# Kernel optimization log

Hardware: AMD Instinct MI355X
Metric: run time of the kernel (lower is better)

Reference implementation:

```python
import jax, jax.numpy as jnp
import numpy as np

HEADS = 8


def setup_inputs() -> dict:
    key = jax.random.key(0)
    k1, k2, k3, k4, k5 = jax.random.split(key, 5)
    bt, b_sz, n, dim = 2, 4, 1024, 512
    inner6 = 3072  # inner_dim * 6 where inner_dim = heads * dim_head = 512
    return {
        "x": jax.random.normal(k1, (bt, b_sz, n, dim), dtype=jnp.float32),
        "W_qkv": jax.random.normal(k2, (dim, inner6), dtype=jnp.float32) * 0.02,
        "b_qkv": jax.random.normal(k3, (inner6,), dtype=jnp.float32) * 0.02,
        "W_out": jax.random.normal(k4, (1024, dim), dtype=jnp.float32) * 0.02,
        "b_out": jax.random.normal(k5, (dim,), dtype=jnp.float32) * 0.02,
    }


def reference(x, W_qkv, b_qkv, W_out, b_out):
    bt, b_sz, n, dim = x.shape
    # to_qkv: Linear(dim, 3072) -> reshape (bt,b,n,3,H,hd) -> transpose(2,4)
    qkv = (x @ W_qkv + b_qkv).reshape(bt, b_sz, n, 3, HEADS, -1)
    qkv = qkv.transpose(0, 1, 4, 3, 2, 5)  # (bt, b, H, 3, n, hd)
    q, k, v = qkv[:, :, :, 0], qkv[:, :, :, 1], qkv[:, :, :, 2]
    scale = (dim // HEADS) ** -0.5  # faithful: uses dim//heads, not per-head width
    attn = jax.nn.softmax(jnp.einsum("abhnd,abhmd->abhnm", q * scale, k), axis=-1)
    out = jnp.einsum("abhnm,abhmd->abhnd", attn, v)
    out = out.transpose(0, 1, 3, 2, 4).reshape(bt, b_sz, n, -1)  # (bt,b,n,H*hd)
    return out @ W_out + b_out
```

## Files before the change

### kernel.cpp

```cpp
#include <hip/hip_runtime.h>

typedef __attribute__((ext_vector_type(4))) float f32x4;
typedef __attribute__((ext_vector_type(16))) float f32x16;
typedef __attribute__((ext_vector_type(8))) __bf16 bf16x8;
typedef __attribute__((ext_vector_type(8))) unsigned short ushortx8;
typedef unsigned short u16;
typedef unsigned int u32;

#define AS1 __attribute__((address_space(1)))
#define AS3 __attribute__((address_space(3)))

__device__ __forceinline__ void gld_lds16(const void* g, void* s) {
  __builtin_amdgcn_global_load_lds((AS1 void*)g, (AS3 void*)s, 16, 0, 0);
}

__device__ __forceinline__ u16 f2bf(float f) {
  unsigned int u = __float_as_uint(f);
  unsigned int r = (u + 0x7FFFu + ((u >> 16) & 1u)) >> 16;
  return (u16)r;
}

#define QSCALE 0.1803368801111244f

__global__ void cvt_f32_bf16(const float* __restrict__ src, u16* __restrict__ dst, int n) {
  int i = (blockIdx.x * blockDim.x + threadIdx.x) * 8;
  if (i >= n) return;
  const float4 a = *(const float4*)&src[i];
  const float4 b = *(const float4*)&src[i + 4];
  ushortx8 o;
  o[0] = f2bf(a.x); o[1] = f2bf(a.y); o[2] = f2bf(a.z); o[3] = f2bf(a.w);
  o[4] = f2bf(b.x); o[5] = f2bf(b.y); o[6] = f2bf(b.z); o[7] = f2bf(b.w);
  *(ushortx8*)&dst[i] = o;
}

__global__ void scale_bias(const float* __restrict__ src, float* __restrict__ dst, int n,
                           int boundary, float s) {
  int i = blockIdx.x * blockDim.x + threadIdx.x;
  if (i < n) dst[i] = src[i] * (i < boundary ? s : 1.0f);
}

__global__ void transpose_to_bf16(const float* __restrict__ src, u16* __restrict__ dst,
                                  int R, int C, int boundary, float s) {
  __shared__ float tile[32][33];
  const int c0 = blockIdx.x * 32, r0 = blockIdx.y * 32;
  const int tx = threadIdx.x, ty = threadIdx.y;
  #pragma unroll
  for (int i = ty; i < 32; i += 8)
    tile[i][tx] = src[(size_t)(r0 + i) * C + c0 + tx];
  __syncthreads();
  #pragma unroll
  for (int i = ty; i < 32; i += 8) {
    const float sc = (c0 + i < boundary) ? s : 1.0f;
    dst[(size_t)(c0 + i) * R + r0 + tx] = f2bf(tile[tx][i] * sc);
  }
}

__global__ void transpose_v(const u16* __restrict__ qkv, u16* __restrict__ vt) {
  __shared__ u16 tile[32][34];
  const int bh = blockIdx.z, b = bh >> 3, h = bh & 7;
  const int n0 = blockIdx.y * 32, d0 = blockIdx.x * 32;
  const int tx = threadIdx.x, ty = threadIdx.y;
  const u16* src = qkv + (size_t)(b * 1024) * 3072 + 2048 + h * 128;
  #pragma unroll
  for (int i = ty; i < 32; i += 8)
    tile[i][tx] = src[(size_t)(n0 + i) * 3072 + d0 + tx];
  __syncthreads();
  u16* dst = vt + (size_t)(b * 8 + h) * 128 * 1024;
  #pragma unroll
  for (int i = ty; i < 32; i += 8)
    dst[(size_t)(d0 + i) * 1024 + n0 + tx] = tile[tx][i];
}

template <int BM, int BN, int BK, int OUT_BF16>
__global__ __launch_bounds__(256, 4) void gemm_bt(const u16* __restrict__ A,
                                                  const u16* __restrict__ Bt,
                                                  const float* __restrict__ bias,
                                                  void* __restrict__ Cv,
                                                  int M, int N, int K) {
  constexpr int RPC = 512 / BK;
  constexpr int LPR = BK / 8;
  constexpr int MASK = LPR - 1;
  constexpr int P = 64 / BK > 0 ? 64 / BK : 1;
  constexpr int CA = BM / RPC, CB = BN / RPC;
  constexpr int CAW = CA / 4, CBW = CB / 4;
  constexpr int VM = CAW + CBW;
  constexpr int FM = BM / 32, FN = BN / 32;
  constexpr int KS = BK / 32;

  __shared__ __attribute__((aligned(16))) u16 As[2][BM * BK];
  __shared__ __attribute__((aligned(16))) u16 Bs[2][BN * BK];
  const int nwg = gridDim.x * gridDim.y;
  int bid = blockIdx.y * gridDim.x + blockIdx.x;
  if ((nwg & 7) == 0) bid = (bid & 7) * (nwg >> 3) + (bid >> 3);
  const int n0 = (bid % gridDim.x) * BN, m0 = (bid / gridDim.x) * BM;
  const int tid = threadIdx.x;
  const int w = tid >> 6, l = tid & 63;
  const int wr = w >> 1, wc = w & 1;
  const int lr = l >> 4, lc = l & 15;
  f32x4 acc[FM][FN] = {};

#define GSTAGE(bi, k0)                                                          \
  do {                                                                          \
    _Pragma("unroll") for (int i = 0; i < CAW; ++i) {                           \
      const int c = w * CAW + i;                                                \
      const int row = c * RPC + l / LPR;                                        \
      const int col = ((l % LPR) ^ ((row / P) & MASK)) * 8;                     \
      gld_lds16(&A[(size_t)(m0 + row) * K + (k0) + col], &As[bi][c * 512]);     \
    }                                                                           \
    _Pragma("unroll") for (int i = 0; i < CBW; ++i) {                           \
      const int c = w * CBW + i;                                                \
      const int row = c * RPC + l / LPR;                                        \
      const int col = ((l % LPR) ^ ((row / P) & MASK)) * 8;                     \
      gld_lds16(&Bt[(size_t)(n0 + row) * K + (k0) + col], &Bs[bi][c * 512]);    \
    }                                                                           \
  } while (0)

#define GCOMP(bi)                                                                      \
  do {                                                                                 \
    _Pragma("unroll") for (int ks = 0; ks < KS; ++ks) {                                \
      bf16x8 af[FM], bfr[FN];                                                          \
      _Pragma("unroll") for (int m = 0; m < FM; ++m) {                                 \
        const int row = wr * (BM / 2) + m * 16 + lc;                                   \
        af[m] = *(const bf16x8*)&As[bi][row * BK +                                     \
                                        (((ks * 4 + lr) ^ ((row / P) & MASK)) << 3)];  \
      }                                                                                \
      _Pragma("unroll") for (int n = 0; n < FN; ++n) {                                 \
        const int row = wc * (BN / 2) + n * 16 + lc;                                   \
        bfr[n] = *(const bf16x8*)&Bs[bi][row * BK +                                    \
                                         (((ks * 4 + lr) ^ ((row / P) & MASK)) << 3)]; \
      }                                                                                \
      __builtin_amdgcn_s_setprio(1);                                                   \
      _Pragma("unroll") for (int m = 0; m < FM; ++m)                                   \
          _Pragma("unroll") for (int n = 0; n < FN; ++n)                               \
              acc[m][n] =                                                              \
          __builtin_amdgcn_mfma_f32_16x16x32_bf16(af[m], bfr[n], acc[m][n], 0, 0, 0);  \
      __builtin_amdgcn_s_setprio(0);                                                   \
    }                                                                                  \
  } while (0)

  GSTAGE(0, 0);
  int buf = 0;
  for (int k0 = BK; k0 < K; k0 += BK) {
    GSTAGE(buf ^ 1, k0);
    if constexpr (VM == 4)
      asm volatile("s_waitcnt vmcnt(4)" ::: "memory");
    else if constexpr (VM == 2)
      asm volatile("s_waitcnt vmcnt(2)" ::: "memory");
    else
      asm volatile("s_waitcnt vmcnt(8)" ::: "memory");
    __builtin_amdgcn_s_barrier();
    __builtin_amdgcn_sched_barrier(0);
    GCOMP(buf);
    __builtin_amdgcn_s_barrier();
    buf ^= 1;
  }
  asm volatile("s_waitcnt vmcnt(0)" ::: "memory");
  __builtin_amdgcn_s_barrier();
  __builtin_amdgcn_sched_barrier(0);
  GCOMP(buf);
#undef GSTAGE
#undef GCOMP

  #pragma unroll
  for (int n = 0; n < FN; ++n) {
    const int col = n0 + wc * (BN / 2) + n * 16 + lc;
    const float bv = bias[col];
    #pragma unroll
    for (int m = 0; m < FM; ++m) {
      #pragma unroll
      for (int r = 0; r < 4; ++r) {
        const int row = m0 + wr * (BM / 2) + m * 16 + lr * 4 + r;
        const float v = acc[m][n][r] + bv;
        if (OUT_BF16)
          ((u16*)Cv)[(size_t)row * N + col] = f2bf(v);
        else
          ((float*)Cv)[(size_t)row * N + col] = v;
      }
    }
  }
}

__global__ __launch_bounds__(256, 2) void attn_fwd(const u16* __restrict__ qkv,
                                                   const u16* __restrict__ vt,
                                                   u16* __restrict__ attn_out) {
  __shared__ __attribute__((aligned(16))) u16 Ks[2][64 * 128];
  __shared__ __attribute__((aligned(16))) u16 Vs[2][64 * 128];
  const int orig = blockIdx.y * 8 + blockIdx.x;
  const int swz = (orig & 7) * 64 + (orig >> 3);
  const int bh = swz >> 3, b = bh >> 3, h = bh & 7;
  const int q0 = (swz & 7) * 128;
  const int tid = threadIdx.x, w = tid >> 6, l = tid & 63;
  const int ll = l & 31, hi = l >> 5;
  const int wq0 = q0 + w * 32;
  const u16* Qb = qkv + (size_t)(b * 1024 + wq0) * 3072 + h * 128;
  const u16* Kb = qkv + (size_t)(b * 1024) * 3072 + 1024 + h * 128;
  const u16* Vb = vt + (size_t)(b * 8 + h) * 128 * 1024;

  bf16x8 bq[8];
  #pragma unroll
  for (int s = 0; s < 8; ++s)
    bq[s] = *(const bf16x8*)&Qb[(size_t)ll * 3072 + s * 16 + hi * 8];
  asm volatile("s_waitcnt vmcnt(0)" ::: "memory");

  bf16x8 ones;
  #pragma unroll
  for (int i = 0; i < 8; ++i) ones[i] = (__bf16)1.0f;

  const u16* sb[8];
  int dst0;
  if (w < 2) {
    #pragma unroll
    for (int j = 0; j < 8; ++j) {
      const int r = w * 32 + j * 4 + (l >> 4);
      const int c = l & 15;
      sb[j] = Kb + (size_t)r * 3072 + ((c ^ (r & 15)) << 3);
    }
    dst0 = w * 4096;
  } else {
    #pragma unroll
    for (int j = 0; j < 8; ++j) {
      const int r2 = (w - 2) * 32 + j * 4 + (l >> 4);
      const int c = l & 15;
      const int d = ((c >> 3) ^ ((r2 >> 3) & 1)) * 64 + (r2 >> 5) * 32 + (r2 & 31);
      const int kc = (c & 7) ^ (r2 & 7);
      sb[j] = Vb + (size_t)d * 1024 + (kc << 3);
    }
    dst0 = (w - 2) * 4096;
  }

#define STAGE(bi, tt)                                                            \
  do {                                                                           \
    if (w < 2) {                                                                 \
      _Pragma("unroll") for (int j = 0; j < 8; ++j)                              \
          gld_lds16(sb[j] + (size_t)(tt)*196608, &Ks[bi][dst0 + j * 512]);       \
    } else {                                                                     \
      _Pragma("unroll") for (int j = 0; j < 8; ++j)                              \
          gld_lds16(sb[j] + (size_t)(tt)*64, &Vs[bi][dst0 + j * 512]);           \
    }                                                                            \
  } while (0)

#define QK(Kt)                                                                     \
  do {                                                                            \
    st0 = (f32x16){};                                                             \
    st1 = (f32x16){};                                                             \
    __builtin_amdgcn_s_setprio(1);                                                \
    _Pragma("unroll") for (int s = 0; s < 8; ++s) {                               \
      const int ch = ((s * 2 + hi) ^ (ll & 15)) << 3;                             \
      const bf16x8 ak0 = *(const bf16x8*)&(Kt)[ll * 128 + ch];                    \
      const bf16x8 ak1 = *(const bf16x8*)&(Kt)[(32 + ll) * 128 + ch];             \
      st0 = __builtin_amdgcn_mfma_f32_32x32x16_bf16(ak0, bq[s], st0, 0, 0, 0);    \
      st1 = __builtin_amdgcn_mfma_f32_32x32x16_bf16(ak1, bq[s], st1, 0, 0, 0);    \
    }                                                                             \
    __builtin_amdgcn_s_setprio(0);                                                \
  } while (0)

#define SOFTMAX()                                                                  \
  do {                                                                            \
    _Pragma("unroll") for (int kb = 0; kb < 2; ++kb) {                            \
      float pe[16];                                                               \
      _Pragma("unroll") for (int r = 0; r < 16; ++r)                              \
          pe[r] = exp2f(kb ? st1[r] : st0[r]);                                    \
      _Pragma("unroll") for (int j = 0; j < 8; ++j) {                             \
        u32 d_;                                                                   \
        asm("v_cvt_pk_bf16_f32 %0, %1, %2"                                        \
            : "=v"(d_)                                                            \
            : "v"(pe[2 * j]), "v"(pe[2 * j + 1]));                                \
        mm[kb * 8 + j] = d_;                                                      \
      }                                                                           \
      asm volatile("v_permlane32_swap_b32 %0, %1"                                 \
                   : "+v"(mm[kb * 8 + 0]), "+v"(mm[kb * 8 + 2]));                 \
      asm volatile("v_permlane32_swap_b32 %0, %1"                                 \
                   : "+v"(mm[kb * 8 + 1]), "+v"(mm[kb * 8 + 3]));                 \
      asm volatile("v_permlane32_swap_b32 %0, %1"                                 \
                   : "+v"(mm[kb * 8 + 4]), "+v"(mm[kb * 8 + 6]));                 \
      asm volatile("v_permlane32_swap_b32 %0, %1"                                 \
                   : "+v"(mm[kb * 8 + 5]), "+v"(mm[kb * 8 + 7]));                 \
    }                                                                             \
  } while (0)

#define PV(Vt_)                                                                    \
  do {                                                                            \
    __builtin_amdgcn_s_setprio(1);                                                \
    _Pragma("unroll") for (int kb = 0; kb < 2; ++kb) {                            \
      _Pragma("unroll") for (int s2 = 0; s2 < 2; ++s2) {                          \
        union { u32 u[4]; bf16x8 v; } pu;                                         \
        pu.u[0] = mm[kb * 8 + s2 * 4 + 0];                                        \
        pu.u[1] = mm[kb * 8 + s2 * 4 + 1];                                        \
        pu.u[2] = mm[kb * 8 + s2 * 4 + 2];                                        \
        pu.u[3] = mm[kb * 8 + s2 * 4 + 3];                                        \
        const bf16x8 pa = pu.v;                                                   \
        acc_l = __builtin_amdgcn_mfma_f32_32x32x16_bf16(pa, ones, acc_l, 0, 0, 0);\
        _Pragma("unroll") for (int db = 0; db < 4; ++db) {                        \
          const int r2 = (db & 1) * 32 + ll;                                      \
          const int c = ((((db >> 1) ^ ((ll >> 3) & 1)) << 3) |                   \
                         ((kb * 4 + s2 * 2 + hi) ^ (ll & 7)));                    \
          const bf16x8 bv = *(const bf16x8*)&(Vt_)[r2 * 128 + c * 8];             \
          acc_o[db] =                                                             \
              __builtin_amdgcn_mfma_f32_32x32x16_bf16(pa, bv, acc_o[db], 0, 0, 0);\
        }                                                                         \
      }                                                                           \
    }                                                                             \
    __builtin_amdgcn_s_setprio(0);                                                \
  } while (0)

  f32x16 acc_o[4] = {};
  f32x16 acc_l = {};
  f32x16 st0, st1;
  u32 mm[16];

  STAGE(0, 0);
  int buf = 0;
  for (int t = 0; t < 15; ++t) {
    STAGE(buf ^ 1, t + 1);
    asm volatile("s_waitcnt vmcnt(8)" ::: "memory");
    __builtin_amdgcn_s_barrier();
    __builtin_amdgcn_sched_barrier(0);
    QK(Ks[buf]);
    SOFTMAX();
    PV(Vs[buf]);
    __builtin_amdgcn_s_barrier();
    buf ^= 1;
  }
  asm volatile("s_waitcnt vmcnt(0)" ::: "memory");
  __builtin_amdgcn_s_barrier();
  __builtin_amdgcn_sched_barrier(0);
  QK(Ks[buf]);
  SOFTMAX();
  PV(Vs[buf]);

#undef STAGE
#undef QK
#undef SOFTMAX
#undef PV

  float inv[16];
  #pragma unroll
  for (int r = 0; r < 16; ++r) inv[r] = __builtin_amdgcn_rcpf(acc_l[r]);
  u16* Ob = attn_out + (size_t)(b * 1024 + wq0) * 1024 + h * 128;
  #pragma unroll
  for (int db = 0; db < 4; ++db)
    #pragma unroll
    for (int r = 0; r < 16; ++r) {
      const int q = (r & 3) + 8 * (r >> 2) + 4 * hi;
      Ob[(size_t)q * 1024 + db * 32 + ll] = f2bf(acc_o[db][r] * inv[r]);
    }
}

extern "C" void kernel_launch(void* const* d_in, const int* in_sizes, int n_in,
                              void* d_out, int out_size, void* d_ws, size_t ws_size,
                              hipStream_t stream) {
  const float* x = (const float*)d_in[0];
  const float* Wqkv = (const float*)d_in[1];
  const float* bqkv = (const float*)d_in[2];
  const float* Wout = (const float*)d_in[3];
  const float* bout = (const float*)d_in[4];
  float* out = (float*)d_out;

  char* ws = (char*)d_ws;
  u16* xb    = (u16*)(ws);
  u16* wqkvt = (u16*)(ws + 8388608);
  u16* woutt = (u16*)(ws + 8388608 + 3145728);
  u16* qkvb  = (u16*)(ws + 12582912);
  u16* vtb   = (u16*)(ws + 62914560);
  u16* aob   = (u16*)(ws + 79691776);
  float* bq2 = (float*)aob;

  cvt_f32_bf16<<<2048, 256, 0, stream>>>(x, xb, 8192 * 512);
  scale_bias<<<12, 256, 0, stream>>>(bqkv, bq2, 3072, 1024, QSCALE);
  transpose_to_bf16<<<dim3(96, 16), dim3(32, 8), 0, stream>>>(Wqkv, wqkvt, 512, 3072, 1024, QSCALE);
  transpose_to_bf16<<<dim3(16, 32), dim3(32, 8), 0, stream>>>(Wout, woutt, 1024, 512, 0, 1.0f);

  gemm_bt<128, 128, 32, 1><<<dim3(24, 64), 256, 0, stream>>>(xb, wqkvt, bq2, qkvb,
                                                             8192, 3072, 512);

  transpose_v<<<dim3(4, 32, 64), dim3(32, 8), 0, stream>>>(qkvb, vtb);

  attn_fwd<<<dim3(8, 64), 256, 0, stream>>>(qkvb, vtb, aob);

  gemm_bt<64, 64, 32, 0><<<dim3(8, 128), 256, 0, stream>>>(aob, woutt, bout, out,
                                                           8192, 512, 1024);
}
```

Baseline: 130.2 us.

## Replace QKV GEMM with 256x192 eight-phase pipelined kernel using swizzled LDS

Adds a dedicated QKV projection GEMM with 256x192 tiles, 8 waves, and a K-step of 64. Global-to-LDS loads are interleaved with MFMA phases across two LDS buffers, using XOR-swizzled layouts to avoid bank conflicts, s_setprio around the MFMA blocks, and a grid remap for L2 locality. The goal is to overlap memory traffic with compute and raise data reuse compared with the generic 128x128 kernel. The cost is large LDS use (112KB per block) and a rigid schedule that assumes K is a multiple of 128 and that M and N divide the tile sizes.

```diff
diff --git a/kernel.cpp b/kernel.cpp
--- a/kernel.cpp
+++ b/kernel.cpp
@@ -175,6 +175,156 @@
           ((u16*)Cv)[(size_t)row * N + col] = f2bf(v);
         else
           ((float*)Cv)[(size_t)row * N + col] = v;
+      }
+    }
+  }
+}
+
+__global__ __launch_bounds__(512, 2) void gemm_qkv_8ph(const u16* __restrict__ A,
+                                                       const u16* __restrict__ Bt,
+                                                       const float* __restrict__ bias,
+                                                       u16* __restrict__ C,
+                                                       int M, int N, int K) {
+  __shared__ __attribute__((aligned(16))) u16 As[2][256 * 64];
+  __shared__ __attribute__((aligned(16))) u16 Bs[2][192 * 64];
+  const int nwg = gridDim.x;
+  int bid = blockIdx.x;
+  if ((nwg & 7) == 0) bid = (bid & 7) * (nwg >> 3) + (bid >> 3);
+  const int ntile = N / 192;
+  const int n0 = (bid % ntile) * 192, m0 = (bid / ntile) * 256;
+  const int tid = threadIdx.x;
+  const int w = tid >> 6, l = tid & 63;
+  const int wr = w >> 2, wc = w & 3;
+  const int lr = l >> 4, lc = l & 15;
+  f32x4 acc[8][3] = {};
+  bf16x8 af[2][2], bfv[3][2];
+
+#define STAGE_A(bi, kt, h)                                                          \
+  do {                                                                              \
+    _Pragma("unroll") for (int cc = 0; cc < 2; ++cc) {                              \
+      const int cib = (h) * 1024 + (cc * 8 + w) * 64;                               \
+      const int ci = cib + l;                                                       \
+      const int row = ci >> 3, ck = ci & 7;                                         \
+      gld_lds16(&A[(size_t)(m0 + row) * K + (kt) * 64 + ((ck ^ (row & 7)) << 3)],   \
+                &As[bi][cib * 8]);                                                  \
+    }                                                                               \
+  } while (0)
+
+#define STAGE_B(bi, kt, t)                                                          \
+  do {                                                                              \
+    const int cib = (t) * 512 + w * 64;                                             \
+    const int ci = cib + l;                                                         \
+    const int row = ci >> 3, ck = ci & 7;                                           \
+    gld_lds16(&Bt[(size_t)(n0 + row) * K + (kt) * 64 + ((ck ^ (row & 7)) << 3)],    \
+              &Bs[bi][cib * 8]);                                                    \
+  } while (0)
+
+#define RD_A(bi, mp)                                                                \
+  do {                                                                              \
+    _Pragma("unroll") for (int m2 = 0; m2 < 2; ++m2)                                \
+      _Pragma("unroll") for (int ks = 0; ks < 2; ++ks) {                            \
+        const int row = wr * 128 + (2 * (mp) + m2) * 16 + lc;                       \
+        af[m2][ks] = *(const bf16x8*)&As[bi][row * 64 +                             \
+                                             (((ks * 4 + lr) ^ (lc & 7)) << 3)];    \
+      }                                                                             \
+  } while (0)
+
+#define RD_B(bi)                                                                    \
+  do {                                                                              \
+    _Pragma("unroll") for (int n = 0; n < 3; ++n)                                   \
+      _Pragma("unroll") for (int ks = 0; ks < 2; ++ks) {                            \
+        const int row = wc * 48 + n * 16 + lc;                                      \
+        bfv[n][ks] = *(const bf16x8*)&Bs[bi][row * 64 +                             \
+                                             (((ks * 4 + lr) ^ (lc & 7)) << 3)];    \
+      }                                                                             \
+  } while (0)
+
+#define MM(mp)                                                                      \
+  do {                                                                              \
+    __builtin_amdgcn_s_setprio(1);                                                  \
+    _Pragma("unroll") for (int m2 = 0; m2 < 2; ++m2)                                \
+      _Pragma("unroll") for (int n = 0; n < 3; ++n)                                 \
+        _Pragma("unroll") for (int ks = 0; ks < 2; ++ks)                            \
+          acc[2 * (mp) + m2][n] = __builtin_amdgcn_mfma_f32_16x16x32_bf16(          \
+              af[m2][ks], bfv[n][ks], acc[2 * (mp) + m2][n], 0, 0, 0);              \
+    __builtin_amdgcn_s_setprio(0);                                                  \
+  } while (0)
+
+#define BARC()                                                                      \
+  do {                                                                              \
+    __builtin_amdgcn_s_barrier();                                                   \
+    asm volatile("s_waitcnt lgkmcnt(0)" ::: "memory");                              \
+    __builtin_amdgcn_sched_barrier(0);                                              \
+  } while (0)
+
+  STAGE_B(0, 0, 0); STAGE_B(0, 0, 1); STAGE_B(0, 0, 2);
+  STAGE_A(0, 0, 0); STAGE_A(0, 0, 1);
+  STAGE_B(1, 1, 0); STAGE_B(1, 1, 1);
+  asm volatile("s_waitcnt vmcnt(2)" ::: "memory");
+  __builtin_amdgcn_s_barrier();
+  __builtin_amdgcn_sched_barrier(0);
+
+  const int NI = K >> 7;
+  for (int i = 0; i < NI; ++i) {
+    const bool nl = (i < NI - 1);
+    const int tO = 2 * i + 1, tE2 = 2 * i + 2, tO2 = 2 * i + 3;
+    RD_B(0); RD_A(0, 0);
+    STAGE_B(1, tO, 2); STAGE_A(1, tO, 0); STAGE_A(1, tO, 1);
+    BARC(); MM(0);
+    __builtin_amdgcn_s_barrier();
+    RD_A(0, 1);
+    if (nl) STAGE_B(0, tE2, 0);
+    BARC(); MM(1);
+    __builtin_amdgcn_s_barrier();
+    RD_A(0, 2);
+    if (nl) STAGE_B(0, tE2, 1);
+    BARC(); MM(2);
+    __builtin_amdgcn_s_barrier();
+    RD_A(0, 3);
+    if (nl) STAGE_B(0, tE2, 2);
+    BARC(); MM(3);
+    if (nl) asm volatile("s_waitcnt vmcnt(3)" ::: "memory");
+    else    asm volatile("s_waitcnt vmcnt(0)" ::: "memory");
+    __builtin_amdgcn_s_barrier();
+    __builtin_amdgcn_sched_barrier(0);
+    RD_B(1); RD_A(1, 0);
+    if (nl) STAGE_A(0, tE2, 0);
+    BARC(); MM(0);
+    __builtin_amdgcn_s_barrier();
+    RD_A(1, 1);
+    if (nl) STAGE_A(0, tE2, 1);
+    BARC(); MM(1);
+    __builtin_amdgcn_s_barrier();
+    RD_A(1, 2);
+    if (nl) STAGE_B(1, tO2, 0);
+    BARC(); MM(2);
+    __builtin_amdgcn_s_barrier();
+    RD_A(1, 3);
+    if (nl) STAGE_B(1, tO2, 1);
+    BARC(); MM(3);
+    if (nl) {
+      asm volatile("s_waitcnt vmcnt(2)" ::: "memory");
+      __builtin_amdgcn_s_barrier();
+      __builtin_amdgcn_sched_barrier(0);
+    }
+  }
+#undef STAGE_A
+#undef STAGE_B
+#undef RD_A
+#undef RD_B
+#undef MM
+#undef BARC
+
+  #pragma unroll
+  for (int n = 0; n < 3; ++n) {
+    const int col = n0 + wc * 48 + n * 16 + lc;
+    const float bv = bias[col];
+    #pragma unroll
+    for (int m = 0; m < 8; ++m) {
+      #pragma unroll
+      for (int r = 0; r < 4; ++r) {
+        const int row = m0 + wr * 128 + m * 16 + lr * 4 + r;
+        C[(size_t)row * N + col] = f2bf(acc[m][n][r] + bv);
       }
     }
   }
@@ -370,8 +520,7 @@
   transpose_to_bf16<<<dim3(96, 16), dim3(32, 8), 0, stream>>>(Wqkv, wqkvt, 512, 3072, 1024, QSCALE);
   transpose_to_bf16<<<dim3(16, 32), dim3(32, 8), 0, stream>>>(Wout, woutt, 1024, 512, 0, 1.0f);
 
-  gemm_bt<128, 128, 32, 1><<<dim3(24, 64), 256, 0, stream>>>(xb, wqkvt, bq2, qkvb,
-                                                             8192, 3072, 512);
+  gemm_qkv_8ph<<<dim3(512), 512, 0, stream>>>(xb, wqkvt, bq2, qkvb, 8192, 3072, 512);
 
   transpose_v<<<dim3(4, 32, 64), dim3(32, 8), 0, stream>>>(qkvb, vtb);
 
```

After: 133.6 us. +2.7%, slower.
